# Kernel optimization log

Measured on AMD Instinct MI355X. Metric: run time of the kernel, lower is better.

## Reference

```python
import jax, jax.numpy as jnp
import numpy as np

M, N, P, T = 8000, 63, 64, 5


def setup_inputs() -> dict:
    key = jax.random.key(0)
    ks = jax.random.split(key, 19)
    sn = (1.0 / N) ** 0.5
    sp = (1.0 / P) ** 0.5
    f32 = jnp.float32
    return {
        "A": jax.random.normal(ks[0], (1, M, N), f32),
        "b": jax.random.normal(ks[1], (1, M), f32),
        "c": jax.random.normal(ks[2], (1, N), f32),
        "theta1r": sn * jax.random.normal(ks[3], (P, N + 1), f32),
        "theta1c": sn * jax.random.normal(ks[4], (P, N + 1), f32),
        "theta2rr": sp * jax.random.normal(ks[5], (P, P), f32),
        "theta2rc": sp * jax.random.normal(ks[6], (P, P), f32),
        "theta2cr": sp * jax.random.normal(ks[7], (P, P), f32),
        "theta3rr": sp * jax.random.normal(ks[8], (P, P), f32),
        "theta3rc": sp * jax.random.normal(ks[9], (P, P), f32),
        "theta3cr": sp * jax.random.normal(ks[10], (P, P), f32),
        "theta4rr": sp * jax.random.normal(ks[11], (P,), f32),
        "theta4rc": sp * jax.random.normal(ks[12], (P,), f32),
        "theta4cr": sp * jax.random.normal(ks[13], (P,), f32),
        "theta6r": sp * jax.random.normal(ks[14], (P, P), f32),
        "theta6c": sp * jax.random.normal(ks[15], (P, P), f32),
        "theta7": sp * jax.random.normal(ks[16], (P, P), f32),
        "W8": 0.05 * jax.random.normal(ks[17], (2, 2 * P), f32),
        "b8": 0.05 * jax.random.normal(ks[18], (2,), f32),
        "z": 7,
    }


def reference(A, b, c, theta1r, theta1c, theta2rr, theta2rc, theta2cr,
              theta3rr, theta3rc, theta3cr, theta4rr, theta4rc, theta4cr,
              theta6r, theta6c, theta7, W8, b8, z):
    relu = jax.nn.relu
    m, n = A.shape[1], A.shape[2]
    p = theta1r.shape[0]
    # raw node features: row node v -> [A[v,:], b[v]]; column node m -> [c, 0]
    Fr_raw = jnp.concatenate([A[0], b[0][:, None]], axis=1)        # (m, n+1)
    fc_raw = jnp.concatenate([c[0], jnp.zeros((1,), A.dtype)])     # (n+1,)
    Fr = Fr_raw / jnp.linalg.norm(Fr_raw, axis=1, keepdims=True)   # f(v), v < m
    fc = fc_raw / jnp.linalg.norm(fc_raw)                          # f(m)
    # edge weights w(v,u) = f(v).f(u) are detached in the original (float(...data))
    Frd = jax.lax.stop_gradient(Fr)
    fcd = jax.lax.stop_gradient(fc)
    Wrr = Frd @ Frd.T                                              # (m, m)
    dg = jnp.diagonal(Wrr)
    srr_pos = relu(Wrr).sum(axis=1) - relu(dg)                     # sum over u != v
    srr_neg = relu(-Wrr).sum(axis=1) - relu(-dg)
    wrc = Frd @ fcd                                                # (m,) = w(v, m)
    # identity: sum_u relu(t4 * w_u) = relu(t4) * sum_u relu(w_u) + relu(-t4) * sum_u relu(-w_u)
    Srr = relu(theta4rr)[:, None] * srr_pos[None, :] + relu(-theta4rr)[:, None] * srr_neg[None, :]
    Src = relu(theta4rc)[:, None] * relu(wrc)[None, :] + relu(-theta4rc)[:, None] * relu(-wrc)[None, :]
    scr = relu(theta4cr) * relu(wrc).sum() + relu(-theta4cr) * relu(-wrc).sum()
    edge_r = theta3rr @ Srr + theta3rc @ Src                       # (p, m), constant over t
    edge_c = theta3cr @ scr                                        # (p,)
    fz = Fr[z]                                                     # z < m: row node feature
    t1r = theta1r @ fz                                             # (p,)
    t1c = theta1c @ fz
    # mu init (p, m+1) = [[Ab^T, c0^T]; 0]; split into row columns / column node
    mu_r0 = jnp.zeros((p, m), A.dtype).at[: n + 1].set(Fr_raw.T)
    mu_c0 = jnp.zeros((p,), A.dtype).at[: n + 1].set(fc_raw)

    def step(carry, _):
        mu_r, mu_c = carry
        # row nodes: term2rr uses old mu[:, v]; term2rc uses old mu[:, m]
        new_r = relu(t1r[:, None] + theta2rr @ mu_r + (theta2rc @ mu_c)[:, None] + edge_r)
        # column node updated last within a sweep -> sees updated row embeddings
        new_c = relu(t1c + theta2cr @ new_r.sum(axis=1) + edge_c)
        return (new_r, new_c), None

    (mu_r, mu_c), _ = jax.lax.scan(step, (mu_r0, mu_c0), None, length=T)
    term6 = theta6r @ mu_r.sum(axis=1) + theta6c @ mu_c            # (p,)
    term7 = theta7 @ mu_r[:, z]                                    # (p,)
    feat = jax.nn.sigmoid(jnp.concatenate([term6, term7]))         # (2p,)
    return (feat @ W8.T + b8)[None, :]                             # (1, 2)
```

## Files before the change

### kernel.cpp

```cpp
#include <hip/hip_runtime.h>
#include <math.h>

typedef __attribute__((ext_vector_type(8))) short short8;
typedef __attribute__((ext_vector_type(4))) float f32x4;

#define WS_SPART 0
#define WS_GPART 262144
#define WS_WPART 294912
#define WS_CPART 295936
#define WS_T1R   336896
#define WS_T1C   336960
#define WS_AL    337024
#define WS_BE    337088
#define WS_GA    337152
#define WS_DE    337216
#define WS_ECP   337280
#define WS_ECN   337344
#define WS_W     337408
#define WS_MUZ   337472
#define WS_WSUM  337536
#define WS_RNORM 337600
#define WS_R2H   345792
#define WS_R2L   347840
#define WS_FLAG  349888
#define WS_GS    350528
#define WS_FH    380928
#define WS_FL    643072

#define NBLK 125

__device__ __forceinline__ float waveReduceSum(float v) {
#pragma unroll
    for (int m = 32; m >= 1; m >>= 1) v += __shfl_xor(v, m, 64);
    return v;
}
__device__ __forceinline__ unsigned short f2bf(float f) {
    unsigned int u = __float_as_uint(f);
    unsigned int r = (u + 0x7fffu + ((u >> 16) & 1u)) >> 16;
    return (unsigned short)r;
}
__device__ __forceinline__ float bf2f(unsigned short h) {
    return __uint_as_float(((unsigned int)h) << 16);
}

__device__ __forceinline__ float sum32_coherent(const float* base) {
    float v[32];
#pragma unroll
    for (int i = 0; i < 32; i++)
        asm volatile("global_load_dword %0, %1, off sc0 sc1"
                     : "=v"(v[i]) : "v"(base + i * 256));
    asm volatile("s_waitcnt vmcnt(0)" ::: "memory");
    __builtin_amdgcn_sched_barrier(0);
    float s = 0.f;
#pragma unroll
    for (int i = 0; i < 32; i++) s += v[i];
    return s;
}

__device__ __forceinline__ void pollFlags(const int* fb, int lane) {
    for (;;) {
        int f0, f1;
        asm volatile("global_load_dword %0, %1, off sc0 sc1"
                     : "=v"(f0) : "v"(fb + lane));
        asm volatile("global_load_dword %0, %1, off sc0 sc1"
                     : "=v"(f1) : "v"(fb + 64 + lane));
        asm volatile("s_waitcnt vmcnt(0)" : "+v"(f0), "+v"(f1) :: "memory");
        __builtin_amdgcn_sched_barrier(0);
        if (__all((f0 == 1) && (f1 == 1))) return;
        __builtin_amdgcn_s_sleep(1);
    }
}

__global__ __launch_bounds__(256) void k_fr(
    const float* __restrict__ A, const float* __restrict__ b, const float* __restrict__ c,
    const float* __restrict__ th1r, const float* __restrict__ th1c,
    const float* __restrict__ th2rr, const float* __restrict__ th2rc,
    const float* __restrict__ th3rr, const float* __restrict__ th3rc, const float* __restrict__ th3cr,
    const float* __restrict__ th4rr, const float* __restrict__ th4rc, const float* __restrict__ th4cr,
    const int* __restrict__ zp,
    unsigned short* __restrict__ Fh, unsigned short* __restrict__ Fl,
    unsigned short* __restrict__ R2H, unsigned short* __restrict__ R2L,
    float* __restrict__ ws)
{
    int tid = threadIdx.x, lane = tid & 63, wid = tid >> 6;

    if (blockIdx.x == 512) {
        __shared__ float fcraw[64], fz[64], sh4a[64], sh4b[64];
        int p = lane;
        int z = zp[0];
        float cv = (p < 63) ? c[p] : 0.f;
        fcraw[p] = cv;
        float av = (p < 63) ? A[z * 63 + p] : b[z];
        float s2 = waveReduceSum(av * av);
        fz[p] = av * rsqrtf(s2);
        __syncthreads();

        float t1 = 0.f, t2 = 0.f, w0 = 0.f;
#pragma unroll 8
        for (int k = 0; k < 64; k++) {
            t1 += th1r[p * 64 + k] * fz[k];
            t2 += th1c[p * 64 + k] * fz[k];
            w0 += th2rc[p * 64 + k] * fcraw[k];
        }
        ws[WS_T1R + p] = t1;
        ws[WS_T1C + p] = t2;
        ws[WS_W + p] = t1 + w0;

        sh4a[p] = th4rr[p];
        sh4b[p] = th4rc[p];
        __syncthreads();
        float a = 0.f, bb = 0.f, g = 0.f, d = 0.f;
#pragma unroll 8
        for (int k = 0; k < 64; k++) {
            float t4 = sh4a[k];
            a  += th3rr[p * 64 + k] * fmaxf(t4, 0.f);
            bb += th3rr[p * 64 + k] * fmaxf(-t4, 0.f);
            float t5 = sh4b[k];
            g  += th3rc[p * 64 + k] * fmaxf(t5, 0.f);
            d  += th3rc[p * 64 + k] * fmaxf(-t5, 0.f);
        }
        ws[WS_AL + p] = a; ws[WS_BE + p] = bb;
        ws[WS_GA + p] = g; ws[WS_DE + p] = d;
        __syncthreads();
        sh4a[p] = th4cr[p];
        __syncthreads();
        float e1 = 0.f, e2 = 0.f;
#pragma unroll 8
        for (int k = 0; k < 64; k++) {
            float t6 = sh4a[k];
            e1 += th3cr[p * 64 + k] * fmaxf(t6, 0.f);
            e2 += th3cr[p * 64 + k] * fmaxf(-t6, 0.f);
        }
        ws[WS_ECP + p] = e1; ws[WS_ECN + p] = e2;

        if (tid < 128) {
            int* fl = (int*)(ws + WS_FLAG);
#pragma unroll
            for (int t5 = 0; t5 < 5; t5++)
                fl[t5 * 128 + tid] = (tid >= NBLK) ? 1 : 0;
        }
        if (tid < 192) {
#pragma unroll
            for (int t5 = 0; t5 < 5; t5++)
                ws[WS_CPART + t5 * 8192 + 8000 + tid] = 0.f;
        }

#pragma unroll
        for (int i = 0; i < 16; i++) {
            int idx = tid * 16 + i;
            float f = th2rr[idx];
            unsigned short h = f2bf(f);
            R2H[idx] = h;
            R2L[idx] = f2bf(f - bf2f(h));
        }
        return;
    }

    __shared__ float gsh[64];
    __shared__ float wsh2[2];
    if (tid < 64) gsh[tid] = 0.f;
    if (tid < 2) wsh2[tid] = 0.f;
    __syncthreads();

    float cv = (lane < 63) ? c[lane] : 0.f;
    float cn2 = waveReduceSum(cv * cv);
    float fcnl = cv * rsqrtf(cn2);

    int r0 = blockIdx.x * 16 + wid * 4;
    float gl = 0.f, lp = 0.f, ln = 0.f;
#pragma unroll
    for (int i = 0; i < 4; i++) {
        int r = r0 + i;
        if (r < 8000) {
            float val = (lane < 63) ? A[r * 63 + lane] : b[r];
            float s2 = waveReduceSum(val * val);
            float f = val * rsqrtf(s2);
            unsigned short h = f2bf(f);
            Fh[r * 64 + lane] = h;
            Fl[r * 64 + lane] = f2bf(f - bf2f(h));
            gl += f;
            float w = waveReduceSum(f * fcnl);
            if (lane == 0) {
                ws[WS_RNORM + r] = sqrtf(s2);
                lp += fmaxf(w, 0.f); ln += fmaxf(-w, 0.f);
            }
        } else {
            Fh[r * 64 + lane] = 0;
            Fl[r * 64 + lane] = 0;
        }
    }
    atomicAdd(&gsh[lane], gl);
    if (lane == 0) { atomicAdd(&wsh2[0], lp); atomicAdd(&wsh2[1], ln); }
    __syncthreads();
    if (tid < 64) ws[WS_GPART + blockIdx.x * 64 + tid] = gsh[tid];
    if (tid == 64) ws[WS_WPART + blockIdx.x * 2 + 0] = wsh2[0];
    if (tid == 65) ws[WS_WPART + blockIdx.x * 2 + 1] = wsh2[1];
}

__global__ __launch_bounds__(256) void k_gram(
    const unsigned short* __restrict__ Fh, float* __restrict__ ws)
{
    __shared__ float red[256];
    __shared__ float colw[4][16][16];
    int tid = threadIdx.x, lane = tid & 63, wid = tid >> 6;
    int m = lane & 15, quad = lane >> 4;
    int tx = blockIdx.x, ty = blockIdx.y;

    if (tx > ty) {
        if (tx == 1 && ty == 0) {
            float gv = 0.f;
#pragma unroll 32
            for (int bb = 0; bb < 128; bb++)
                gv += ws[WS_GPART + (wid * 128 + bb) * 64 + lane];
            red[tid] = gv;
            if (wid == 1) {
                float wp = 0.f;
#pragma unroll
                for (int k = 0; k < 8; k++) wp += ws[WS_WPART + (lane + 64 * k) * 2];
                wp = waveReduceSum(wp);
                if (lane == 0) ws[WS_WSUM] = wp;
            } else if (wid == 2) {
                float wn = 0.f;
#pragma unroll
                for (int k = 0; k < 8; k++) wn += ws[WS_WPART + (lane + 64 * k) * 2 + 1];
                wn = waveReduceSum(wn);
                if (lane == 0) ws[WS_WSUM + 1] = wn;
            }
            __syncthreads();
            if (tid < 64)
                ws[WS_GS + tid] = red[tid] + red[64 + tid] + red[128 + tid] + red[192 + tid];
        }
        return;
    }

    int vbase = tx * 256 + wid * 64;
    int ubase = ty * 256;

    short8 AH[8];
#pragma unroll
    for (int pt = 0; pt < 4; pt++)
#pragma unroll
        for (int q = 0; q < 2; q++)
            AH[pt * 2 + q] = *(const short8*)(Fh + (vbase + pt * 16 + m) * 64 + q * 32 + quad * 8);

    float srr[16];
#pragma unroll
    for (int i = 0; i < 16; i++) srr[i] = 0.f;

    const int boff = m * 64 + quad * 8;
    const int ub = ubase * 64;
    short8 B0[2], B1[2];
#pragma unroll
    for (int q = 0; q < 2; q++)
        B0[q] = *(const short8*)(Fh + ub + boff + q * 32);

#pragma unroll 1
    for (int k2 = 0; k2 < 8; k2++) {
#pragma unroll
        for (int q = 0; q < 2; q++)
            B1[q] = *(const short8*)(Fh + ub + (2 * k2 + 1) * 1024 + boff + q * 32);
        {
            float cs = 0.f;
#pragma unroll
            for (int pt = 0; pt < 4; pt++) {
                f32x4 a = {0.f, 0.f, 0.f, 0.f};
                a = __builtin_amdgcn_mfma_f32_16x16x32_bf16(AH[pt * 2 + 0], B0[0], a, 0, 0, 0);
                a = __builtin_amdgcn_mfma_f32_16x16x32_bf16(AH[pt * 2 + 1], B0[1], a, 0, 0, 0);
#pragma unroll
                for (int r = 0; r < 4; r++) {
                    float rr = fmaxf(a[r], 0.f);
                    srr[pt * 4 + r] += rr; cs += rr;
                }
            }
            cs += __shfl_xor(cs, 16, 64);
            cs += __shfl_xor(cs, 32, 64);
            if (quad == 0) colw[wid][2 * k2][m] = cs;
        }
        if (k2 < 7)
#pragma unroll
            for (int q = 0; q < 2; q++)
                B0[q] = *(const short8*)(Fh + ub + (2 * k2 + 2) * 1024 + boff + q * 32);
        {
            float cs = 0.f;
#pragma unroll
            for (int pt = 0; pt < 4; pt++) {
                f32x4 a = {0.f, 0.f, 0.f, 0.f};
                a = __builtin_amdgcn_mfma_f32_16x16x32_bf16(AH[pt * 2 + 0], B1[0], a, 0, 0, 0);
                a = __builtin_amdgcn_mfma_f32_16x16x32_bf16(AH[pt * 2 + 1], B1[1], a, 0, 0, 0);
#pragma unroll
                for (int r = 0; r < 4; r++) {
                    float rr = fmaxf(a[r], 0.f);
                    srr[pt * 4 + r] += rr; cs += rr;
                }
            }
            cs += __shfl_xor(cs, 16, 64);
            cs += __shfl_xor(cs, 32, 64);
            if (quad == 0) colw[wid][2 * k2 + 1][m] = cs;
        }
    }
    __syncthreads();
#pragma unroll
    for (int pt = 0; pt < 4; pt++)
#pragma unroll
        for (int r = 0; r < 4; r++) {
            float s = srr[pt * 4 + r];
            s += __shfl_xor(s, 1, 64); s += __shfl_xor(s, 2, 64);
            s += __shfl_xor(s, 4, 64); s += __shfl_xor(s, 8, 64);
            if (m == 0)
                ws[WS_SPART + ty * 8192 + vbase + pt * 16 + quad * 4 + r] = s;
        }
    if (tx < ty) {
        float csum = colw[0][tid >> 4][tid & 15] + colw[1][tid >> 4][tid & 15]
                   + colw[2][tid >> 4][tid & 15] + colw[3][tid >> 4][tid & 15];
        ws[WS_SPART + tx * 8192 + ubase + tid] = csum;
    }
}

__global__ __launch_bounds__(256) void k_mu_fused(
    const float* __restrict__ c,
    const float* __restrict__ th2cr, const float* __restrict__ th2rc,
    const float* __restrict__ th6r, const float* __restrict__ th6c,
    const float* __restrict__ th7, const float* __restrict__ W8,
    const float* __restrict__ b8, const int* __restrict__ zp,
    float* __restrict__ ws,
    const unsigned short* __restrict__ Fh, const unsigned short* __restrict__ Fl,
    const unsigned short* __restrict__ R2H, const unsigned short* __restrict__ R2L,
    float* __restrict__ out)
{
    __shared__ float XF[64][68];
    __shared__ unsigned short UHT[64][72], ULT[64][72];
    __shared__ float red[256], colp[256];
    __shared__ __align__(16) float wS[64], alS[64], beS[64], gaS[64], deS[64];
    __shared__ float fcnS[64], gS[64], sprow[64];
    __shared__ __align__(16) float e4sh[256];
    __shared__ float Ssh[64], ysh[64], feat[128], muzS[64];

    int tid = threadIdx.x, lane = tid & 63, wid = tid >> 6;
    int m = lane & 15, quad = lane >> 4;
    int v0 = blockIdx.x * 64;
    int cw = wid * 16 + m;
    int v = v0 + cw;
    int z = zp[0];
    int* flags = (int*)(ws + WS_FLAG);

    short8 RH[8], RL[8];
#pragma unroll
    for (int pt = 0; pt < 4; pt++)
#pragma unroll
        for (int q = 0; q < 2; q++) {
            int off = (pt * 16 + m) * 64 + q * 32 + quad * 8;
            RH[pt * 2 + q] = *(const short8*)(R2H + off);
            RL[pt * 2 + q] = *(const short8*)(R2L + off);
        }

    int prow = wid * 16 + m;
    float4 Tcr[4], Trc[4];
#pragma unroll
    for (int kk = 0; kk < 4; kk++) {
        Tcr[kk] = ((const float4*)(th2cr + prow * 64 + quad * 16))[kk];
        Trc[kk] = ((const float4*)(th2rc + prow * 64 + quad * 16))[kk];
    }
    float t1c_r = ws[WS_T1C + prow], t1r_r = ws[WS_T1R + prow];
    float ecp_r = ws[WS_ECP + prow], ecn_r = ws[WS_ECN + prow];
    float wsp = ws[WS_WSUM], wsn = ws[WS_WSUM + 1];

    if (wid == 0) {
        float cv = (lane < 63) ? c[lane] : 0.f;
        float cn2 = waveReduceSum(cv * cv);
        fcnS[lane] = cv * rsqrtf(cn2);
        wS[lane] = ws[WS_W + lane];
    } else if (wid == 1) {
        alS[lane] = ws[WS_AL + lane]; beS[lane] = ws[WS_BE + lane];
    } else if (wid == 2) {
        gaS[lane] = ws[WS_GA + lane]; deS[lane] = ws[WS_DE + lane];
    } else {
        gS[lane] = ws[WS_GS + lane];
    }
    float sv = 0.f;
#pragma unroll
    for (int y = wid * 8; y < wid * 8 + 8; y++) sv += ws[WS_SPART + y * 8192 + v0 + lane];
    red[tid] = sv;
    __syncthreads();
    if (tid < 64) sprow[tid] = red[tid] + red[64 + tid] + red[128 + tid] + red[192 + tid];
    __syncthreads();

    for (int i2 = 0; i2 < 16; i2++) {
        int i = wid * 16 + i2;
        int vr = v0 + i;
        float fr = bf2f(Fh[vr * 64 + lane]) + bf2f(Fl[vr * 64 + lane]);
        float dw = waveReduceSum(fr * fcnS[lane]);
        float dg = waveReduceSum(fr * gS[lane]);
        if (lane == 0) {
            float spv = sprow[i];
            float4 ee;
            ee.x = spv - 1.0f;
            ee.y = spv - dg;
            ee.z = fmaxf(dw, 0.f);
            ee.w = fmaxf(-dw, 0.f);
            *(float4*)(&e4sh[i * 4]) = ee;
        }
        XF[i][lane] = fr * ws[WS_RNORM + vr];
    }
    __syncthreads();

    short8 BH[2], BL[2];
#pragma unroll
    for (int q = 0; q < 2; q++) {
        float4 f0 = *(const float4*)(&XF[cw][q * 32 + quad * 8]);
        float4 f1 = *(const float4*)(&XF[cw][q * 32 + quad * 8 + 4]);
        float xv[8] = {f0.x, f0.y, f0.z, f0.w, f1.x, f1.y, f1.z, f1.w};
        short8 H, L;
#pragma unroll
        for (int j = 0; j < 8; j++) {
            unsigned short h = f2bf(xv[j]);
            H[j] = (short)h;
            L[j] = (short)f2bf(xv[j] - bf2f(h));
        }
        BH[q] = H; BL[q] = L;
    }
    float4 e = *(const float4*)(&e4sh[cw * 4]);

    for (int t = 0; t < 5; t++) {
        if (t > 0) {
#pragma unroll
            for (int q = 0; q < 2; q++) {
                BH[q] = *(const short8*)(&UHT[cw][q * 32 + quad * 8]);
                BL[q] = *(const short8*)(&ULT[cw][q * 32 + quad * 8]);
            }
        }
        f32x4 acc[4];
#pragma unroll
        for (int pt = 0; pt < 4; pt++) {
            f32x4 a = {0.f, 0.f, 0.f, 0.f};
#pragma unroll
            for (int q = 0; q < 2; q++) {
                a = __builtin_amdgcn_mfma_f32_16x16x32_bf16(RH[pt*2+q], BH[q], a, 0, 0, 0);
                a = __builtin_amdgcn_mfma_f32_16x16x32_bf16(RH[pt*2+q], BL[q], a, 0, 0, 0);
                a = __builtin_amdgcn_mfma_f32_16x16x32_bf16(RL[pt*2+q], BH[q], a, 0, 0, 0);
            }
            acc[pt] = a;
        }

        if (t > 0) {
            if (wid == 0) pollFlags(flags + (t - 1) * 128, lane);
            __syncthreads();
            red[tid] = sum32_coherent(ws + WS_CPART + (t - 1) * 8192 + wid * 64 + lane);
            __syncthreads();
            if (tid < 64) Ssh[tid] = red[tid] + red[64 + tid] + red[128 + tid] + red[192 + tid];
            __syncthreads();
            {
                float acc2 = 0.f;
#pragma unroll
                for (int kk = 0; kk < 4; kk++) {
                    float4 r4 = Tcr[kk];
                    acc2 += r4.x * Ssh[quad * 16 + 4 * kk]     + r4.y * Ssh[quad * 16 + 4 * kk + 1]
                          + r4.z * Ssh[quad * 16 + 4 * kk + 2] + r4.w * Ssh[quad * 16 + 4 * kk + 3];
                }
                acc2 += __shfl_xor(acc2, 16, 64);
                acc2 += __shfl_xor(acc2, 32, 64);
                if (quad == 0)
                    ysh[prow] = fmaxf(acc2 + t1c_r + wsp * ecp_r + wsn * ecn_r, 0.f);
            }
            __syncthreads();
            {
                float acc2 = 0.f;
#pragma unroll
                for (int kk = 0; kk < 4; kk++) {
                    float4 r4 = Trc[kk];
                    acc2 += r4.x * ysh[quad * 16 + 4 * kk]     + r4.y * ysh[quad * 16 + 4 * kk + 1]
                          + r4.z * ysh[quad * 16 + 4 * kk + 2] + r4.w * ysh[quad * 16 + 4 * kk + 3];
                }
                acc2 += __shfl_xor(acc2, 16, 64);
                acc2 += __shfl_xor(acc2, 32, 64);
                if (quad == 0) wS[prow] = acc2 + t1r_r;
            }
            __syncthreads();
        }

#pragma unroll
        for (int pt = 0; pt < 4; pt++) {
            f32x4 a = acc[pt];
            int pbase = pt * 16 + quad * 4;
            float4 w4 = *(const float4*)(wS + pbase);
            float4 a4 = *(const float4*)(alS + pbase);
            float4 b4 = *(const float4*)(beS + pbase);
            float4 g4 = *(const float4*)(gaS + pbase);
            float4 d4 = *(const float4*)(deS + pbase);
            float u0 = fmaxf(a[0] + w4.x + a4.x*e.x + b4.x*e.y + g4.x*e.z + d4.x*e.w, 0.f);
            float u1 = fmaxf(a[1] + w4.y + a4.y*e.x + b4.y*e.y + g4.y*e.z + d4.y*e.w, 0.f);
            float u2 = fmaxf(a[2] + w4.z + a4.z*e.x + b4.z*e.y + g4.z*e.z + d4.z*e.w, 0.f);
            float u3 = fmaxf(a[3] + w4.w + a4.w*e.x + b4.w*e.y + g4.w*e.z + d4.w*e.w, 0.f);
            if (t < 4) {
                ushort4 h4, l4;
                h4.x = f2bf(u0); l4.x = f2bf(u0 - bf2f(h4.x));
                h4.y = f2bf(u1); l4.y = f2bf(u1 - bf2f(h4.y));
                h4.z = f2bf(u2); l4.z = f2bf(u2 - bf2f(h4.z));
                h4.w = f2bf(u3); l4.w = f2bf(u3 - bf2f(h4.w));
                *(ushort4*)(&UHT[cw][pbase]) = h4;
                *(ushort4*)(&ULT[cw][pbase]) = l4;
            } else if (v == z) {
                __hip_atomic_store(&ws[WS_MUZ + pbase + 0], u0, __ATOMIC_RELAXED, __HIP_MEMORY_SCOPE_AGENT);
                __hip_atomic_store(&ws[WS_MUZ + pbase + 1], u1, __ATOMIC_RELAXED, __HIP_MEMORY_SCOPE_AGENT);
                __hip_atomic_store(&ws[WS_MUZ + pbase + 2], u2, __ATOMIC_RELAXED, __HIP_MEMORY_SCOPE_AGENT);
                __hip_atomic_store(&ws[WS_MUZ + pbase + 3], u3, __ATOMIC_RELAXED, __HIP_MEMORY_SCOPE_AGENT);
            }
            float c0 = u0, c1 = u1, c2 = u2, c3 = u3;
#pragma unroll
            for (int mm = 1; mm < 16; mm <<= 1) {
                c0 += __shfl_xor(c0, mm, 64);
                c1 += __shfl_xor(c1, mm, 64);
                c2 += __shfl_xor(c2, mm, 64);
                c3 += __shfl_xor(c3, mm, 64);
            }
            if (m == 0) {
                colp[wid * 64 + pbase + 0] = c0;
                colp[wid * 64 + pbase + 1] = c1;
                colp[wid * 64 + pbase + 2] = c2;
                colp[wid * 64 + pbase + 3] = c3;
            }
        }
        __syncthreads();
        if (tid < 64)
            __hip_atomic_store(&ws[WS_CPART + t * 8192 + blockIdx.x * 64 + tid],
                               colp[tid] + colp[64 + tid] + colp[128 + tid] + colp[192 + tid],
                               __ATOMIC_RELAXED, __HIP_MEMORY_SCOPE_AGENT);
        __syncthreads();
        if (tid == 0) {
            asm volatile("s_waitcnt vmcnt(0)" ::: "memory");
            __hip_atomic_store(&flags[t * 128 + (int)blockIdx.x], 1,
                               __ATOMIC_RELAXED, __HIP_MEMORY_SCOPE_AGENT);
        }
    }

    if (blockIdx.x != 0) return;

    if (wid == 0) pollFlags(flags + 4 * 128, lane);
    __syncthreads();

    red[tid] = sum32_coherent(ws + WS_CPART + 4 * 8192 + wid * 64 + lane);
    if (tid < 64) {
        float mz;
        asm volatile("global_load_dword %0, %1, off sc0 sc1"
                     : "=v"(mz) : "v"(ws + WS_MUZ + tid));
        asm volatile("s_waitcnt vmcnt(0)" : "+v"(mz) :: "memory");
        __builtin_amdgcn_sched_barrier(0);
        muzS[tid] = mz;
    }
    __syncthreads();
    if (tid < 64) Ssh[tid] = red[tid] + red[64 + tid] + red[128 + tid] + red[192 + tid];
    __syncthreads();
    int p = tid;
    if (p < 64) {
        float acc2 = ws[WS_T1C + p] + ws[WS_WSUM] * ws[WS_ECP + p]
                   + ws[WS_WSUM + 1] * ws[WS_ECN + p];
#pragma unroll 8
        for (int k = 0; k < 64; k++) acc2 += th2cr[p * 64 + k] * Ssh[k];
        ysh[p] = fmaxf(acc2, 0.f);
    }
    __syncthreads();
    if (p < 64) {
        float t6 = 0.f, t7 = 0.f;
#pragma unroll 8
        for (int k = 0; k < 64; k++) {
            t6 += th6r[p * 64 + k] * Ssh[k] + th6c[p * 64 + k] * ysh[k];
            t7 += th7[p * 64 + k] * muzS[k];
        }
        feat[p] = 1.f / (1.f + expf(-t6));
        feat[64 + p] = 1.f / (1.f + expf(-t7));
    }
    __syncthreads();
    if (p < 2) {
        float o = b8[p];
        for (int i = 0; i < 128; i++) o += W8[p * 128 + i] * feat[i];
        out[p] = o;
    }
}

extern "C" void kernel_launch(void* const* d_in, const int* in_sizes, int n_in,
                              void* d_out, int out_size, void* d_ws, size_t ws_size,
                              hipStream_t stream) {
    (void)in_sizes; (void)n_in; (void)out_size; (void)ws_size;
    const float* A     = (const float*)d_in[0];
    const float* b     = (const float*)d_in[1];
    const float* c     = (const float*)d_in[2];
    const float* th1r  = (const float*)d_in[3];
    const float* th1c  = (const float*)d_in[4];
    const float* th2rr = (const float*)d_in[5];
    const float* th2rc = (const float*)d_in[6];
    const float* th2cr = (const float*)d_in[7];
    const float* th3rr = (const float*)d_in[8];
    const float* th3rc = (const float*)d_in[9];
    const float* th3cr = (const float*)d_in[10];
    const float* th4rr = (const float*)d_in[11];
    const float* th4rc = (const float*)d_in[12];
    const float* th4cr = (const float*)d_in[13];
    const float* th6r  = (const float*)d_in[14];
    const float* th6c  = (const float*)d_in[15];
    const float* th7   = (const float*)d_in[16];
    const float* W8    = (const float*)d_in[17];
    const float* b8    = (const float*)d_in[18];
    const int*   zp    = (const int*)d_in[19];
    float* ws  = (float*)d_ws;
    float* out = (float*)d_out;
    unsigned short* Fh  = (unsigned short*)(ws + WS_FH);
    unsigned short* Fl  = (unsigned short*)(ws + WS_FL);
    unsigned short* R2H = (unsigned short*)(ws + WS_R2H);
    unsigned short* R2L = (unsigned short*)(ws + WS_R2L);

    k_fr<<<513, 256, 0, stream>>>(A, b, c, th1r, th1c, th2rr, th2rc, th3rr, th3rc,
                                  th3cr, th4rr, th4rc, th4cr, zp, Fh, Fl, R2H, R2L, ws);
    k_gram<<<dim3(32, 32), 256, 0, stream>>>(Fh, ws);
    {
        const unsigned short* Fhc = Fh;
        const unsigned short* Flc = Fl;
        const unsigned short* R2Hc = R2H;
        const unsigned short* R2Lc = R2L;
        void* kargs[] = {
            (void*)&c, (void*)&th2cr, (void*)&th2rc, (void*)&th6r, (void*)&th6c,
            (void*)&th7, (void*)&W8, (void*)&b8, (void*)&zp, (void*)&ws,
            (void*)&Fhc, (void*)&Flc, (void*)&R2Hc, (void*)&R2Lc, (void*)&out };
        hipLaunchCooperativeKernel((const void*)k_mu_fused, dim3(NBLK), dim3(256),
                                   kargs, 0, stream);
    }
}
```

Before: 218.4 us.

## Have one block reduce column partials and broadcast the result via a flag

```diff
diff --git a/kernel.cpp b/kernel.cpp
--- a/kernel.cpp
+++ b/kernel.cpp
@@ -24,6 +24,8 @@
 #define WS_R2L   347840
 #define WS_FLAG  349888
 #define WS_GS    350528
+#define WS_PUB   350592
+#define WS_WG    350720
 #define WS_FH    380928
 #define WS_FL    643072
 
@@ -67,6 +69,18 @@
         asm volatile("s_waitcnt vmcnt(0)" : "+v"(f0), "+v"(f1) :: "memory");
         __builtin_amdgcn_sched_barrier(0);
         if (__all((f0 == 1) && (f1 == 1))) return;
+        __builtin_amdgcn_s_sleep(1);
+    }
+}
+
+__device__ __forceinline__ void pollOne(const int* pw) {
+    for (;;) {
+        int f;
+        asm volatile("global_load_dword %0, %1, off sc0 sc1"
+                     : "=v"(f) : "v"(pw));
+        asm volatile("s_waitcnt vmcnt(0)" : "+v"(f) :: "memory");
+        __builtin_amdgcn_sched_barrier(0);
+        if (__all(f == 1)) return;
         __builtin_amdgcn_s_sleep(1);
     }
 }
@@ -139,6 +153,7 @@
             for (int t5 = 0; t5 < 5; t5++)
                 fl[t5 * 128 + tid] = (tid >= NBLK) ? 1 : 0;
         }
+        if (tid < 80) ((int*)(ws + WS_PUB))[tid] = 0;
         if (tid < 192) {
 #pragma unroll
             for (int t5 = 0; t5 < 5; t5++)
@@ -342,6 +357,7 @@
     int v = v0 + cw;
     int z = zp[0];
     int* flags = (int*)(ws + WS_FLAG);
+    int* pub   = (int*)(ws + WS_PUB);
 
     short8 RH[8], RL[8];
 #pragma unroll
@@ -442,39 +458,62 @@
         }
 
         if (t > 0) {
-            if (wid == 0) pollFlags(flags + (t - 1) * 128, lane);
-            __syncthreads();
-            red[tid] = sum32_coherent(ws + WS_CPART + (t - 1) * 8192 + wid * 64 + lane);
-            __syncthreads();
-            if (tid < 64) Ssh[tid] = red[tid] + red[64 + tid] + red[128 + tid] + red[192 + tid];
-            __syncthreads();
-            {
-                float acc2 = 0.f;
-#pragma unroll
-                for (int kk = 0; kk < 4; kk++) {
-                    float4 r4 = Tcr[kk];
-                    acc2 += r4.x * Ssh[quad * 16 + 4 * kk]     + r4.y * Ssh[quad * 16 + 4 * kk + 1]
-                          + r4.z * Ssh[quad * 16 + 4 * kk + 2] + r4.w * Ssh[quad * 16 + 4 * kk + 3];
+            if (blockIdx.x == 0) {
+                if (wid == 0) pollFlags(flags + (t - 1) * 128, lane);
+                __syncthreads();
+                red[tid] = sum32_coherent(ws + WS_CPART + (t - 1) * 8192 + wid * 64 + lane);
+                __syncthreads();
+                if (tid < 64) Ssh[tid] = red[tid] + red[64 + tid] + red[128 + tid] + red[192 + tid];
+                __syncthreads();
+                {
+                    float acc2 = 0.f;
+#pragma unroll
+                    for (int kk = 0; kk < 4; kk++) {
+                        float4 r4 = Tcr[kk];
+                        acc2 += r4.x * Ssh[quad * 16 + 4 * kk]     + r4.y * Ssh[quad * 16 + 4 * kk + 1]
+                              + r4.z * Ssh[quad * 16 + 4 * kk + 2] + r4.w * Ssh[quad * 16 + 4 * kk + 3];
+                    }
+                    acc2 += __shfl_xor(acc2, 16, 64);
+                    acc2 += __shfl_xor(acc2, 32, 64);
+                    if (quad == 0)
+                        ysh[prow] = fmaxf(acc2 + t1c_r + wsp * ecp_r + wsn * ecn_r, 0.f);
                 }
-                acc2 += __shfl_xor(acc2, 16, 64);
-                acc2 += __shfl_xor(acc2, 32, 64);
-                if (quad == 0)
-                    ysh[prow] = fmaxf(acc2 + t1c_r + wsp * ecp_r + wsn * ecn_r, 0.f);
-            }
-            __syncthreads();
-            {
-                float acc2 = 0.f;
-#pragma unroll
-                for (int kk = 0; kk < 4; kk++) {
-                    float4 r4 = Trc[kk];
-                    acc2 += r4.x * ysh[quad * 16 + 4 * kk]     + r4.y * ysh[quad * 16 + 4 * kk + 1]
-                          + r4.z * ysh[quad * 16 + 4 * kk + 2] + r4.w * ysh[quad * 16 + 4 * kk + 3];
+                __syncthreads();
+                {
+                    float acc2 = 0.f;
+#pragma unroll
+                    for (int kk = 0; kk < 4; kk++) {
+                        float4 r4 = Trc[kk];
+                        acc2 += r4.x * ysh[quad * 16 + 4 * kk]     + r4.y * ysh[quad * 16 + 4 * kk + 1]
+                              + r4.z * ysh[quad * 16 + 4 * kk + 2] + r4.w * ysh[quad * 16 + 4 * kk + 3];
+                    }
+                    acc2 += __shfl_xor(acc2, 16, 64);
+                    acc2 += __shfl_xor(acc2, 32, 64);
+                    if (quad == 0) wS[prow] = acc2 + t1r_r;
                 }
-                acc2 += __shfl_xor(acc2, 16, 64);
-                acc2 += __shfl_xor(acc2, 32, 64);
-                if (quad == 0) wS[prow] = acc2 + t1r_r;
-            }
-            __syncthreads();
+                __syncthreads();
+                if (tid < 64)
+                    __hip_atomic_store(&ws[WS_WG + (t - 1) * 64 + tid], wS[tid],
+                                       __ATOMIC_RELAXED, __HIP_MEMORY_SCOPE_AGENT);
+                __syncthreads();
+                if (tid == 0) {
+                    asm volatile("s_waitcnt vmcnt(0)" ::: "memory");
+                    __hip_atomic_store(&pub[(t - 1) * 16], 1,
+                                       __ATOMIC_RELAXED, __HIP_MEMORY_SCOPE_AGENT);
+                }
+            } else {
+                if (wid == 0) pollOne(pub + (t - 1) * 16);
+                __syncthreads();
+                if (tid < 64) {
+                    float wv;
+                    asm volatile("global_load_dword %0, %1, off sc0 sc1"
+                                 : "=v"(wv) : "v"(ws + WS_WG + (t - 1) * 64 + tid));
+                    asm volatile("s_waitcnt vmcnt(0)" : "+v"(wv) :: "memory");
+                    __builtin_amdgcn_sched_barrier(0);
+                    wS[tid] = wv;
+                }
+                __syncthreads();
+            }
         }
 
 #pragma unroll
```

Result: slower. 224.8 us (+2.9%).
